# Kernel tuning notes

Hardware: AMD Instinct MI355X
Metric: run time of the kernel (lower is better)

The kernel has to match this reference:

```python
import jax, jax.numpy as jnp
import numpy as np

L, B, E, H, HID = 2048, 4, 512, 8, 2048
HD = E // H


def setup_inputs() -> dict:
    key = jax.random.key(0)
    ks = jax.random.split(key, 6)
    s = 0.02
    x = jax.random.normal(ks[0], (L, B, E), jnp.float32)
    in_proj_w = jax.random.normal(ks[1], (3 * E, E), jnp.float32) * s
    in_proj_b = jnp.zeros((3 * E,), jnp.float32)
    out_w = jax.random.normal(ks[2], (E, E), jnp.float32) * s
    out_b = jnp.zeros((E,), jnp.float32)
    w1 = jax.random.normal(ks[3], (HID, E), jnp.float32) * s  # torch Linear: (out, in)
    b1 = jnp.zeros((HID,), jnp.float32)
    w2 = jax.random.normal(ks[4], (E, HID), jnp.float32) * s
    b2 = jnp.zeros((E,), jnp.float32)
    ln_g = jnp.ones((E,), jnp.float32)
    ln_b = jnp.zeros((E,), jnp.float32)
    return {"x": x, "in_proj_w": in_proj_w, "in_proj_b": in_proj_b,
            "out_w": out_w, "out_b": out_b, "w1": w1, "b1": b1,
            "w2": w2, "b2": b2, "ln_g": ln_g, "ln_b": ln_b}


def _pos_encoding(S, Emb, dtype):
    # even i: sin((t+1) * 10000^(-i/E)); odd i: cos((t+1) * 10000^(-(i+1)/E))
    t = jnp.arange(S, dtype=dtype)[:, None]
    i = jnp.arange(Emb, dtype=dtype)[None, :]
    even = jnp.sin((t + 1.0) * jnp.power(10000.0, -i / Emb))
    odd = jnp.cos((t + 1.0) * jnp.power(10000.0, -(i + 1.0) / Emb))
    return jnp.where(jnp.arange(Emb)[None, :] % 2 == 0, even, odd)  # (S, Emb)


def _layernorm(x, g, b, eps=1e-5):
    mu = jnp.mean(x, axis=-1, keepdims=True)
    var = jnp.mean(jnp.square(x - mu), axis=-1, keepdims=True)
    return (x - mu) * jax.lax.rsqrt(var + eps) * g + b


def _mha(x, in_proj_w, in_proj_b, out_w, out_b):
    # x: (L, B, E); self-attention, torch MultiheadAttention semantics
    qkv = jnp.einsum('lbe,fe->lbf', x, in_proj_w) + in_proj_b
    q, k, v = jnp.split(qkv, 3, axis=-1)
    q = q.reshape(L, B, H, HD)
    k = k.reshape(L, B, H, HD)
    v = v.reshape(L, B, H, HD)
    scores = jnp.einsum('lbhd,mbhd->bhlm', q, k) / np.sqrt(HD).astype(np.float32)
    attn = jax.nn.softmax(scores, axis=-1)
    o = jnp.einsum('bhlm,mbhd->lbhd', attn, v).reshape(L, B, E)
    return jnp.einsum('lbe,fe->lbf', o, out_w) + out_b


def reference(x, in_proj_w, in_proj_b, out_w, out_b, w1, b1, w2, b2, ln_g, ln_b):
    # positional encoding: varies along dim1, broadcasts along dim0 (as in source)
    pe = _pos_encoding(x.shape[1], x.shape[2], x.dtype)  # (B, E)
    x = x + pe[None, :, :]
    # Post-Norm path
    x = _layernorm(_mha(x, in_proj_w, in_proj_b, out_w, out_b) + x, ln_g, ln_b)
    h = jax.nn.gelu(jnp.einsum('lbe,he->lbh', x, w1) + b1, approximate=False)
    ff = jnp.einsum('lbh,eh->lbe', h, w2) + b2
    x = _layernorm(ff + x, ln_g, ln_b)
    return x
```

## Files before the change

kernel.cpp:

```cpp
#include <hip/hip_runtime.h>

typedef unsigned short u16;
typedef unsigned int   u32;
typedef u16  u16x2 __attribute__((ext_vector_type(2)));
typedef u16  u16x4 __attribute__((ext_vector_type(4)));
typedef u16  u16x8 __attribute__((ext_vector_type(8)));
typedef short s8v  __attribute__((ext_vector_type(8)));
typedef float f4v  __attribute__((ext_vector_type(4)));
typedef u32  u32x2 __attribute__((ext_vector_type(2)));
typedef u32  u32x4 __attribute__((ext_vector_type(4)));

#define L_SEQ 2048
#define B_SZ  4
#define E_DIM 512
#define H_CNT 8
#define HD    64
#define HID   2048
#define M_ROWS (L_SEQ * B_SZ)
#define QSCALE 0.18033688011112042f

__device__ __forceinline__ u16 f2b(float f) {
    unsigned u = __builtin_bit_cast(unsigned, f);
    u += 0x7fffu + ((u >> 16) & 1u);
    return (u16)(u >> 16);
}
__device__ __forceinline__ float b2f(u16 u) {
    u32 x = ((u32)u) << 16; return __builtin_bit_cast(float, x);
}
#if defined(__has_builtin)
#if __has_builtin(__builtin_amdgcn_cvt_pk_bf16_f32)
#define HAVE_PK_BF16 1
#endif
#if __has_builtin(__builtin_amdgcn_rcpf)
#define HAVE_RCPF 1
#endif
#endif
__device__ __forceinline__ u32 pk_trunc(float a, float b) {
#ifdef HAVE_PK_BF16
    typedef __bf16 bf2 __attribute__((ext_vector_type(2)));
    bf2 r = __builtin_amdgcn_cvt_pk_bf16_f32(a, b);
    return __builtin_bit_cast(u32, r);
#else
    u32 ua = __builtin_bit_cast(u32, a), ub = __builtin_bit_cast(u32, b);
    return (ua >> 16) | (ub & 0xffff0000u);
#endif
}
__device__ __forceinline__ float frcp(float x) {
#ifdef HAVE_RCPF
    return __builtin_amdgcn_rcpf(x);
#else
    return 1.0f / x;
#endif
}
__device__ __forceinline__ void gload_lds16(const u16* g, u16* l) {
    __builtin_amdgcn_global_load_lds((__attribute__((address_space(1))) void*)(u16*)g,
                                     (__attribute__((address_space(3))) void*)l, 16, 0, 0);
}
__device__ __forceinline__ float gelu_f(float v) {
    float y2 = v * (1.5957691216f + 0.0713548576f * v * v);
    return v / (1.0f + __expf(-y2));
}

__global__ __launch_bounds__(256) void pe_tab_k(float* __restrict__ pet) {
    int i = blockIdx.x * 256 + threadIdx.x;
    int e = i & (E_DIM - 1);
    float t = (float)(i >> 9) + 1.0f;
    int ee = (e & 1) ? (e + 1) : e;
    float w = exp2f((-(float)ee / 512.0f) * 13.287712379549449f);
    pet[i] = (e & 1) ? cosf(t * w) : sinf(t * w);
}

__global__ __launch_bounds__(256) void pe_add_k(const float* __restrict__ x,
                                                const float* __restrict__ pet,
                                                u16* __restrict__ xpb) {
    int idx = (blockIdx.x * 256 + threadIdx.x) * 4;
    f4v v = *(const f4v*)(x + idx);
    f4v p = *(const f4v*)(pet + (idx & 2047));
    u16x4 o;
#pragma unroll
    for (int i = 0; i < 4; ++i) o[i] = f2b(v[i] + p[i]);
    *(u16x4*)(xpb + idx) = o;
}

__global__ __launch_bounds__(256) void conv4_k(const float* __restrict__ s1, u16* __restrict__ d1, int n1,
                                               const float* __restrict__ s2, u16* __restrict__ d2, int n2,
                                               const float* __restrict__ s3, u16* __restrict__ d3, int n3,
                                               const float* __restrict__ s4, u16* __restrict__ d4) {
    int o = (blockIdx.x * 256 + threadIdx.x) * 4;
    const float* s; u16* d;
    if (o < n1) { s = s1; d = d1; }
    else { o -= n1;
        if (o < n2) { s = s2; d = d2; }
        else { o -= n2;
            if (o < n3) { s = s3; d = d3; }
            else { o -= n3; s = s4; d = d4; } } }
    f4v v = *(const f4v*)(s + o);
    u16x4 q;
#pragma unroll
    for (int i = 0; i < 4; ++i) q[i] = f2b(v[i]);
    *(u16x4*)(d + o) = q;
}

template <int NP, bool WRITEF, bool WRITEB>
__global__ __launch_bounds__(256)
void ln_c(const u16* __restrict__ p0, const u16* __restrict__ p1,
          const u16* __restrict__ p2, const u16* __restrict__ p3,
          const float* __restrict__ bias, const u16* __restrict__ resid,
          const float* __restrict__ gw, const float* __restrict__ bw,
          float* __restrict__ outF, u16* __restrict__ outB) {
    int wave = threadIdx.x >> 6, lane = threadIdx.x & 63;
    size_t row = (size_t)blockIdx.x * 4 + wave;
    size_t off = row * E_DIM + lane * 8;
    u16x8 rv = *(const u16x8*)(resid + off);
    f4v a, b;
#pragma unroll
    for (int i = 0; i < 4; ++i) { a[i] = b2f(rv[i]); b[i] = b2f(rv[i + 4]); }
    a += *(const f4v*)(bias + lane * 8);
    b += *(const f4v*)(bias + lane * 8 + 4);
    const u16* ps[4] = {p0, p1, p2, p3};
#pragma unroll
    for (int z = 0; z < NP; ++z) {
        u16x8 t = *(const u16x8*)(ps[z] + off);
#pragma unroll
        for (int i = 0; i < 4; ++i) { a[i] += b2f(t[i]); b[i] += b2f(t[i + 4]); }
    }
    float s = (a[0] + a[1]) + (a[2] + a[3]) + (b[0] + b[1]) + (b[2] + b[3]);
#pragma unroll
    for (int o = 1; o < 64; o <<= 1) s += __shfl_xor(s, o, 64);
    float mu = s * (1.0f / E_DIM);
    float q = 0.f;
#pragma unroll
    for (int i = 0; i < 4; ++i) { float d = a[i] - mu; q += d * d; }
#pragma unroll
    for (int i = 0; i < 4; ++i) { float d = b[i] - mu; q += d * d; }
#pragma unroll
    for (int o = 1; o < 64; o <<= 1) q += __shfl_xor(q, o, 64);
    float rstd = rsqrtf(q * (1.0f / E_DIM) + 1e-5f);
    f4v g0 = *(const f4v*)(gw + lane * 8), g1 = *(const f4v*)(gw + lane * 8 + 4);
    f4v w0 = *(const f4v*)(bw + lane * 8), w1 = *(const f4v*)(bw + lane * 8 + 4);
    f4v y0, y1;
#pragma unroll
    for (int i = 0; i < 4; ++i) { y0[i] = (a[i] - mu) * rstd * g0[i] + w0[i];
                                  y1[i] = (b[i] - mu) * rstd * g1[i] + w1[i]; }
    if (WRITEF) {
        *(f4v*)(outF + off)     = y0;
        *(f4v*)(outF + off + 4) = y1;
    }
    if (WRITEB) {
        u16x8 o;
#pragma unroll
        for (int i = 0; i < 4; ++i) { o[i] = f2b(y0[i]); o[i + 4] = f2b(y1[i]); }
        *(u16x8*)(outB + off) = o;
    }
}

__global__ __launch_bounds__(256) void transpose_v_k(const u16* __restrict__ vb,
                                                     u16* __restrict__ vt) {
    __shared__ __align__(16) u16 T[64 * 66];
    int t = threadIdx.x;
    int lt = blockIdx.x, bh = blockIdx.y;
    const u16* src = vb + (size_t)bh * (L_SEQ * HD) + (size_t)lt * 64 * HD;
    int lr = t >> 2, d0 = (t & 3) * 16;
    s8v va = *(const s8v*)(src + lr * HD + d0);
    s8v vb8 = *(const s8v*)(src + lr * HD + d0 + 8);
#pragma unroll
    for (int c = 0; c < 4; ++c) {
        u16x2 p0; p0[0] = (u16)va[c * 2]; p0[1] = (u16)va[c * 2 + 1];
        u16x2 p1; p1[0] = (u16)vb8[c * 2]; p1[1] = (u16)vb8[c * 2 + 1];
        *(u16x2*)(&T[lr * 66 + d0 + c * 2])     = p0;
        *(u16x2*)(&T[lr * 66 + d0 + 8 + c * 2]) = p1;
    }
    __syncthreads();
    int d = t >> 2, l0 = (t & 3) * 16;
    u16 tmp[16];
#pragma unroll
    for (int i = 0; i < 16; ++i) tmp[i] = T[(l0 + i) * 66 + d];
    u16* dst = vt + (size_t)bh * (L_SEQ * HD) + (size_t)d * L_SEQ + lt * 64 + l0;
    u16x8 o0, o1;
#pragma unroll
    for (int i = 0; i < 8; ++i) { o0[i] = tmp[i]; o1[i] = tmp[8 + i]; }
    *(u16x8*)dst       = o0;
    *(u16x8*)(dst + 8) = o1;
}

template <int MODE, int NT>
__global__ __launch_bounds__(256, 4)
void gemm_bt(const u16* __restrict__ A, const u16* __restrict__ Bw,
             const float* __restrict__ bias, int M, int N, int K,
             u16* __restrict__ outB,
             u16* __restrict__ oq, u16* __restrict__ okk, u16* __restrict__ ov) {
    __shared__ __align__(16) u16 As[2][128 * 32];
    __shared__ __align__(16) u16 Bs[2][128 * 32];
    const int tid = threadIdx.x;
    const int wave = tid >> 6, lane = tid & 63;
    const int col = lane & 15, quad = lane >> 4;
    const int n = blockIdx.x;
    const int xcd = n & 7, loc = n >> 3;
    const int mpx = (M / 128) >> 3;
    const int bm = (xcd * mpx + loc / NT) * 128;
    const int bn = (loc % NT) * 128;
    const int wm = (wave >> 1) * 64, wn = (wave & 1) * 64;
    f4v acc[4][4] = {};
    const int srow = wave * 16 + (lane >> 2);
    const int soff = (lane & 3) * 8;
    const u16* Ag = A + (size_t)(bm + srow) * K + soff;
    const u16* Bg = Bw + (size_t)(bn + srow) * K + soff;
    const int wo = wave * 512;
    gload_lds16(Ag,                  &As[0][wo]);
    gload_lds16(Ag + (size_t)64 * K, &As[0][wo + 2048]);
    gload_lds16(Bg,                  &Bs[0][wo]);
    gload_lds16(Bg + (size_t)64 * K, &Bs[0][wo + 2048]);
    const int nit = K >> 5;
    for (int t = 0; t < nit; ++t) {
        const int cur = t & 1, nxt = cur ^ 1;
        __syncthreads();
        if (t + 1 < nit) {
            const int kc = (t + 1) * 32;
            gload_lds16(Ag + kc,                  &As[nxt][wo]);
            gload_lds16(Ag + (size_t)64 * K + kc, &As[nxt][wo + 2048]);
            gload_lds16(Bg + kc,                  &Bs[nxt][wo]);
            gload_lds16(Bg + (size_t)64 * K + kc, &Bs[nxt][wo + 2048]);
        }
        s8v af[4], bf[4];
#pragma unroll
        for (int i = 0; i < 4; ++i) af[i] = *(const s8v*)(&As[cur][(wm + i * 16 + col) * 32 + quad * 8]);
#pragma unroll
        for (int j = 0; j < 4; ++j) bf[j] = *(const s8v*)(&Bs[cur][(wn + j * 16 + col) * 32 + quad * 8]);
#pragma unroll
        for (int i = 0; i < 4; ++i)
#pragma unroll
            for (int j = 0; j < 4; ++j)
                acc[i][j] = __builtin_amdgcn_mfma_f32_16x16x32_bf16(af[i], bf[j], acc[i][j], 0, 0, 0);
    }
#pragma unroll
    for (int j = 0; j < 4; ++j) {
        int gn = bn + wn + j * 16 + col;
        float bv = bias[gn];
        int which = gn >> 9, hh = (gn >> 6) & 7, d = gn & 63;
        u16* dst = (MODE == 0) ? ((which == 0) ? oq : ((which == 1) ? okk : ov)) : outB;
        float qs = (MODE == 0 && which == 0) ? QSCALE : 1.0f;
#pragma unroll
        for (int i = 0; i < 4; ++i) {
            int gm0 = bm + wm + i * 16 + quad * 4;
#pragma unroll
            for (int r = 0; r < 4; ++r) {
                float v = acc[i][j][r] + bv;
                int m = gm0 + r;
                if (MODE == 2) {
                    outB[(size_t)m * N + gn] = f2b(gelu_f(v));
                } else {
                    int l = m >> 2, bb = m & 3;
                    dst[((size_t)(bb * H_CNT + hh) * L_SEQ + l) * HD + d] = f2b(v * qs);
                }
            }
        }
    }
}

__global__ __launch_bounds__(256, 4)
void gemm_ks(const u16* __restrict__ A, const u16* __restrict__ Bw,
             int N, int K, int Kper,
             u16* __restrict__ q0, u16* __restrict__ q1) {
    __shared__ __align__(16) u16 As[2][128 * 32];
    __shared__ __align__(16) u16 Bs[2][128 * 32];
    const int tid = threadIdx.x;
    const int wave = tid >> 6, lane = tid & 63;
    const int col = lane & 15, quad = lane >> 4;
    const int n = blockIdx.x;
    const int xcd = n & 7, loc = n >> 3;
    const int bn = (loc & 3) * 128;
    const int bm = (xcd * 8 + ((loc >> 2) & 7)) * 128;
    const int kz = loc >> 5;
    u16* pz = kz ? q1 : q0;
    const int wm = (wave >> 1) * 64, wn = (wave & 1) * 64;
    f4v acc[4][4] = {};
    const int srow = wave * 16 + (lane >> 2);
    const int soff = (lane & 3) * 8;
    const u16* Ag = A + (size_t)(bm + srow) * K + kz * Kper + soff;
    const u16* Bg = Bw + (size_t)(bn + srow) * K + kz * Kper + soff;
    const int wo = wave * 512;
    gload_lds16(Ag,                  &As[0][wo]);
    gload_lds16(Ag + (size_t)64 * K, &As[0][wo + 2048]);
    gload_lds16(Bg,                  &Bs[0][wo]);
    gload_lds16(Bg + (size_t)64 * K, &Bs[0][wo + 2048]);
    const int nit = Kper >> 5;
    for (int t = 0; t < nit; ++t) {
        const int cur = t & 1, nxt = cur ^ 1;
        __syncthreads();
        if (t + 1 < nit) {
            const int kc = (t + 1) * 32;
            gload_lds16(Ag + kc,                  &As[nxt][wo]);
            gload_lds16(Ag + (size_t)64 * K + kc, &As[nxt][wo + 2048]);
            gload_lds16(Bg + kc,                  &Bs[nxt][wo]);
            gload_lds16(Bg + (size_t)64 * K + kc, &Bs[nxt][wo + 2048]);
        }
        s8v af[4], bf[4];
#pragma unroll
        for (int i = 0; i < 4; ++i) af[i] = *(const s8v*)(&As[cur][(wm + i * 16 + col) * 32 + quad * 8]);
#pragma unroll
        for (int j = 0; j < 4; ++j) bf[j] = *(const s8v*)(&Bs[cur][(wn + j * 16 + col) * 32 + quad * 8]);
#pragma unroll
        for (int i = 0; i < 4; ++i)
#pragma unroll
            for (int j = 0; j < 4; ++j)
                acc[i][j] = __builtin_amdgcn_mfma_f32_16x16x32_bf16(af[i], bf[j], acc[i][j], 0, 0, 0);
    }
#pragma unroll
    for (int j = 0; j < 4; ++j) {
        int gn = bn + wn + j * 16 + col;
#pragma unroll
        for (int i = 0; i < 4; ++i) {
            int m0 = bm + wm + i * 16 + quad * 4;
#pragma unroll
            for (int r = 0; r < 4; ++r)
                pz[(size_t)(m0 + r) * N + gn] = f2b(acc[i][j][r]);
        }
    }
}

__global__ __launch_bounds__(256, 4)
void attn_k(const u16* __restrict__ qg, const u16* __restrict__ kg,
            const u16* __restrict__ vtg, u16* __restrict__ og) {
    __shared__ __align__(16) u16 Ks[2][2][64 * 32];
    __shared__ __align__(16) u16 Vs[2][2][64 * 32];
    const int tid = threadIdx.x;
    const int wave = tid >> 6, lane = tid & 63;
    const int col = lane & 15, quad = lane >> 4;
    const int flat = blockIdx.x;
    const int xcd = flat & 7, loc = flat >> 3;
    const int bh = xcd * 4 + (loc >> 4);
    const int qc = loc & 15;
    const size_t base = (size_t)bh * (L_SEQ * HD);
    s8v qf[2][2];
#pragma unroll
    for (int t = 0; t < 2; ++t) {
        const int qrow = qc * 128 + wave * 32 + t * 16 + col;
#pragma unroll
        for (int hh = 0; hh < 2; ++hh)
            qf[t][hh] = *(const s8v*)(qg + base + (size_t)qrow * HD + hh * 32 + quad * 8);
    }
    f4v oa[2][4] = {};
    float ls0 = 0.f, ls1 = 0.f;
    const int h = wave & 1, r0 = (wave >> 1) * 16;
    const int srow = lane >> 2, c = lane & 3;
    const int cp = c ^ ((srow >> 1) & 3);
    const int sig = ((srow >> 2) << 3) + ((r0 >> 4) << 2) + (srow & 3);
    const u16* Kg = kg + base + (size_t)sig * HD + h * 32 + cp * 8;
    const u16* Vg = vtg + base + (size_t)(r0 + srow) * L_SEQ + h * 32 + cp * 8;
    {
        gload_lds16(Kg,                      &Ks[0][h][r0 * 32]);
        gload_lds16(Kg + (size_t)32 * HD,    &Ks[0][h][(r0 + 32) * 32]);
        gload_lds16(Vg,                      &Vs[0][h][r0 * 32]);
        gload_lds16(Vg + (size_t)32 * L_SEQ, &Vs[0][h][(r0 + 32) * 32]);
    }
    const int perm = (col >> 1) & 3;
    for (int it = 0; it < 32; ++it) {
        const int cur = it & 1, nxt = cur ^ 1;
        __syncthreads();
        if (it + 1 < 32) {
            const int kv0 = (it + 1) * 64;
            gload_lds16(Kg + (size_t)kv0 * HD,         &Ks[nxt][h][r0 * 32]);
            gload_lds16(Kg + (size_t)(kv0 + 32) * HD,  &Ks[nxt][h][(r0 + 32) * 32]);
            gload_lds16(Vg + kv0,                      &Vs[nxt][h][r0 * 32]);
            gload_lds16(Vg + kv0 + (size_t)32 * L_SEQ, &Vs[nxt][h][(r0 + 32) * 32]);
        }
        f4v st[2][4];
#pragma unroll
        for (int j = 0; j < 4; ++j) {
            s8v k0 = *(const s8v*)(&Ks[cur][0][(j * 16 + col) * 32 + ((quad ^ perm) * 8)]);
            s8v k1 = *(const s8v*)(&Ks[cur][1][(j * 16 + col) * 32 + ((quad ^ perm) * 8)]);
#pragma unroll
            for (int t = 0; t < 2; ++t) {
                f4v z = {};
                z = __builtin_amdgcn_mfma_f32_16x16x32_bf16(k0, qf[t][0], z, 0, 0, 0);
                z = __builtin_amdgcn_mfma_f32_16x16x32_bf16(k1, qf[t][1], z, 0, 0, 0);
                st[t][j] = z;
            }
        }
        u32 pk[2][4][2];
#pragma unroll
        for (int t = 0; t < 2; ++t)
#pragma unroll
            for (int j = 0; j < 4; ++j) {
                f4v p;
#pragma unroll
                for (int r = 0; r < 4; ++r) p[r] = __builtin_amdgcn_exp2f(st[t][j][r]);
                float psum = (p[0] + p[1]) + (p[2] + p[3]);
                if (t == 0) ls0 += psum; else ls1 += psum;
                pk[t][j][0] = pk_trunc(p[0], p[1]);
                pk[t][j][1] = pk_trunc(p[2], p[3]);
            }
#pragma unroll
        for (int c2 = 0; c2 < 2; ++c2) {
            s8v pf[2];
#pragma unroll
            for (int t = 0; t < 2; ++t) {
                u32x4 q4 = {pk[t][2 * c2][0], pk[t][2 * c2][1],
                            pk[t][2 * c2 + 1][0], pk[t][2 * c2 + 1][1]};
                pf[t] = __builtin_bit_cast(s8v, q4);
            }
#pragma unroll
            for (int dj = 0; dj < 4; ++dj) {
                s8v vf = *(const s8v*)(&Vs[cur][c2][(dj * 16 + col) * 32 + ((quad ^ perm) * 8)]);
#pragma unroll
                for (int t = 0; t < 2; ++t)
                    oa[t][dj] = __builtin_amdgcn_mfma_f32_16x16x32_bf16(pf[t], vf, oa[t][dj], 0, 0, 0);
            }
        }
    }
    ls0 += __shfl_xor(ls0, 16, 64); ls0 += __shfl_xor(ls0, 32, 64);
    ls1 += __shfl_xor(ls1, 16, 64); ls1 += __shfl_xor(ls1, 32, 64);
    const int b = bh >> 3, hd = bh & 7;
#pragma unroll
    for (int t = 0; t < 2; ++t)
#pragma unroll
        for (int r = 0; r < 4; ++r) {
            float lv = __shfl(t == 0 ? ls0 : ls1, quad * 4 + r, 64);
            float inv = frcp(lv);
            int lrow = qc * 128 + wave * 32 + t * 16 + quad * 4 + r;
            size_t mrow = (size_t)(lrow * 4 + b) * E_DIM + hd * HD;
#pragma unroll
            for (int dj = 0; dj < 4; ++dj)
                og[mrow + dj * 16 + col] = f2b(oa[t][dj][r] * inv);
        }
}

extern "C" void kernel_launch(void* const* d_in, const int* in_sizes, int n_in,
                              void* d_out, int out_size, void* d_ws, size_t ws_size,
                              hipStream_t stream) {
    const float* x     = (const float*)d_in[0];
    const float* w_qkv = (const float*)d_in[1];
    const float* b_qkv = (const float*)d_in[2];
    const float* w_out = (const float*)d_in[3];
    const float* b_out = (const float*)d_in[4];
    const float* w1    = (const float*)d_in[5];
    const float* b1    = (const float*)d_in[6];
    const float* w2    = (const float*)d_in[7];
    const float* b2    = (const float*)d_in[8];
    const float* ln_g  = (const float*)d_in[9];
    const float* ln_b  = (const float*)d_in[10];

    char* ws = (char*)d_ws;
    u16*   WQKV = (u16*)(ws + 0);
    u16*   WOUT = (u16*)(ws + 1572864);
    u16*   W1B  = (u16*)(ws + 2097152);
    u16*   W2B  = (u16*)(ws + 4194304);
    u16*   XPB  = (u16*)(ws + 6291456);
    u16*   QB   = (u16*)(ws + 14680064);
    u16*   KB   = (u16*)(ws + 23068672);
    u16*   VB   = (u16*)(ws + 31457280);
    u16*   VT   = (u16*)(ws + 39845888);
    float* PET  = (float*)(ws + 82837504);
    u16*   OB   = VB;
    u16*   OP0  = (u16*)(ws + 48234496);
    u16*   OP1  = (u16*)(ws + 56623104);
    u16*   X3B  = QB;
    u16*   HB   = (u16*)(ws + 48234496);
    u16*   FP0  = XPB;
    u16*   FP1  = KB;

    pe_tab_k<<<8, 256, 0, stream>>>(PET);
    pe_add_k<<<4096, 256, 0, stream>>>(x, PET, XPB);
    conv4_k<<<3072, 256, 0, stream>>>(w_qkv, WQKV, 3 * E_DIM * E_DIM,
                                      w_out, WOUT, E_DIM * E_DIM,
                                      w1, W1B, HID * E_DIM,
                                      w2, W2B);
    gemm_bt<0, 12><<<768, 256, 0, stream>>>(XPB, WQKV, b_qkv, M_ROWS, 3 * E_DIM, E_DIM,
                                            nullptr, QB, KB, VB);
    transpose_v_k<<<dim3(32, 32), 256, 0, stream>>>(VB, VT);
    attn_k<<<512, 256, 0, stream>>>(QB, KB, VT, OB);
    gemm_ks<<<512, 256, 0, stream>>>(OB, WOUT, E_DIM, E_DIM, 256, OP0, OP1);
    ln_c<2, false, true><<<2048, 256, 0, stream>>>(OP0, OP1, nullptr, nullptr,
                                                   b_out, XPB, ln_g, ln_b, nullptr, X3B);
    gemm_bt<2, 16><<<1024, 256, 0, stream>>>(X3B, W1B, b1, M_ROWS, HID, E_DIM,
                                             HB, nullptr, nullptr, nullptr);
    gemm_ks<<<512, 256, 0, stream>>>(HB, W2B, E_DIM, HID, 1024, FP0, FP1);
    ln_c<2, true, false><<<2048, 256, 0, stream>>>(FP0, FP1, nullptr, nullptr,
                                                   b2, X3B, ln_g, ln_b, (float*)d_out, nullptr);
}
```

Before: 243.4 us.

## Add 256x256 eight-wave triple-buffered GEMM for FFN layers with 4-way split-K

Introduces a new 512-thread GEMM kernel with 256x256 output tiles, triple-buffered direct global-to-LDS loads with swizzling, and MFMA priority hints. It replaces the FFN up-projection (with fused GELU) and the down-projection, which now uses a 4-way K split whose partial sums are combined in the layernorm kernel. The aim is more data reuse per tile and better overlap of loads with compute. The cost is larger LDS use (96KB dynamic), fewer blocks, and an extra partial buffer to read in the final layernorm.

Result: slower. 249.5 us (+2.5%).

```diff
diff --git a/kernel.cpp b/kernel.cpp
--- a/kernel.cpp
+++ b/kernel.cpp
@@ -318,6 +318,103 @@
     }
 }
 
+#define G8_STAGE(Ad, Bd, kf)                                                           \
+    {                                                                                  \
+        _Pragma("unroll")                                                              \
+        for (int s = 0; s < 2; ++s) {                                                  \
+            const int q = (s * 8 + wave) * 64 + lane;                                  \
+            const int rho = q >> 2;                                                    \
+            gload_lds16(A  + (size_t)(bm + rho) * Ka + (kf) + gsw, (Ad) + q * 8);      \
+            gload_lds16(Bw + (size_t)(bn + rho) * Kb + (kf) + gsw, (Bd) + q * 8);      \
+        }                                                                              \
+    }
+
+#define G8_COMPUTE(Ab_, Bb_)                                                           \
+    {                                                                                  \
+        s8v bfr[4];                                                                    \
+        _Pragma("unroll")                                                              \
+        for (int j = 0; j < 4; ++j) {                                                  \
+            const int rB = wc * 64 + j * 16 + col;                                     \
+            bfr[j] = *(const s8v*)((Bb_) + rB * 32 + ((quad ^ ((rB >> 1) & 3)) * 8));  \
+        }                                                                              \
+        _Pragma("unroll")                                                              \
+        for (int ih = 0; ih < 2; ++ih) {                                               \
+            s8v afr[4];                                                                \
+            _Pragma("unroll")                                                          \
+            for (int i = 0; i < 4; ++i) {                                              \
+                const int rA = wr * 128 + (ih * 4 + i) * 16 + col;                     \
+                afr[i] = *(const s8v*)((Ab_) + rA * 32 + ((quad ^ ((rA >> 1) & 3)) * 8)); \
+            }                                                                          \
+            __builtin_amdgcn_s_setprio(1);                                             \
+            _Pragma("unroll")                                                          \
+            for (int i = 0; i < 4; ++i)                                                \
+                _Pragma("unroll")                                                      \
+                for (int j = 0; j < 4; ++j)                                            \
+                    acc[ih * 4 + i][j] = __builtin_amdgcn_mfma_f32_16x16x32_bf16(afr[i], bfr[j], acc[ih * 4 + i][j], 0, 0, 0); \
+            __builtin_amdgcn_s_setprio(0);                                             \
+        }                                                                              \
+    }
+
+template <int MODE, int NTL, int KZL>
+__global__ __launch_bounds__(512, 2)
+void gemm8(const u16* __restrict__ A, const u16* __restrict__ Bw,
+           const float* __restrict__ bias, int Ka, int Kb, int N,
+           u16* __restrict__ o0, u16* __restrict__ o1,
+           u16* __restrict__ o2, u16* __restrict__ o3) {
+    extern __shared__ __align__(16) u16 LDS[];
+    const int tid = threadIdx.x;
+    const int wave = tid >> 6, lane = tid & 63;
+    const int col = lane & 15, quad = lane >> 4;
+    const int wr = wave >> 2, wc = wave & 3;
+    const int n = blockIdx.x;
+    const int xcd = n & 7, loc = n >> 3;
+    const int mt = xcd * 4 + (loc & 3);
+    const int rest = loc >> 2;
+    const int nt = (NTL == 1) ? 0 : (rest % NTL);
+    const int kz = (KZL == 1) ? 0 : (rest / NTL);
+    const int bm = mt * 256, bn = nt * 256;
+    const int koff0 = kz * 512;
+    const int gsw = ((lane & 3) ^ ((lane >> 3) & 3)) * 8;
+    f4v acc[8][4] = {};
+    u16* A0 = LDS;          u16* B0 = LDS + 8192;
+    u16* A1 = LDS + 16384;  u16* B1 = LDS + 24576;
+    u16* A2 = LDS + 32768;  u16* B2 = LDS + 40960;
+    G8_STAGE(A0, B0, koff0);
+    G8_STAGE(A1, B1, koff0 + 32);
+    asm volatile("s_waitcnt vmcnt(4)" ::: "memory");
+    __builtin_amdgcn_s_barrier();
+    __builtin_amdgcn_sched_barrier(0);
+    for (int t = 0; t < 14; ++t) {
+        G8_STAGE(A2, B2, koff0 + (t + 2) * 32);
+        G8_COMPUTE(A0, B0);
+        asm volatile("s_waitcnt vmcnt(4)" ::: "memory");
+        __builtin_amdgcn_s_barrier();
+        __builtin_amdgcn_sched_barrier(0);
+        u16* ta = A0; A0 = A1; A1 = A2; A2 = ta;
+        u16* tb = B0; B0 = B1; B1 = B2; B2 = tb;
+    }
+    G8_COMPUTE(A0, B0);
+    asm volatile("s_waitcnt vmcnt(0)" ::: "memory");
+    __builtin_amdgcn_s_barrier();
+    __builtin_amdgcn_sched_barrier(0);
+    G8_COMPUTE(A1, B1);
+    u16* outp = (MODE == 2) ? o0 : ((kz == 0) ? o0 : (kz == 1) ? o1 : (kz == 2) ? o2 : o3);
+#pragma unroll
+    for (int j = 0; j < 4; ++j) {
+        const int gn = bn + wc * 64 + j * 16 + col;
+        const float bv = (MODE == 2) ? bias[gn] : 0.0f;
+#pragma unroll
+        for (int i = 0; i < 8; ++i) {
+            const int m0 = bm + wr * 128 + i * 16 + quad * 4;
+#pragma unroll
+            for (int r = 0; r < 4; ++r) {
+                float v = acc[i][j][r] + bv;
+                outp[(size_t)(m0 + r) * N + gn] = f2b(MODE == 2 ? gelu_f(v) : v);
+            }
+        }
+    }
+}
+
 __global__ __launch_bounds__(256, 4)
 void attn_k(const u16* __restrict__ qg, const u16* __restrict__ kg,
             const u16* __restrict__ vtg, u16* __restrict__ og) {
@@ -458,6 +555,17 @@
     u16*   HB   = (u16*)(ws + 48234496);
     u16*   FP0  = XPB;
     u16*   FP1  = KB;
+    u16*   FP2  = VB;
+    u16*   FP3  = VT;
+
+    static bool attr_done = false;
+    if (!attr_done) {
+        hipFuncSetAttribute((const void*)gemm8<2, 8, 1>,
+                            hipFuncAttributeMaxDynamicSharedMemorySize, 98304);
+        hipFuncSetAttribute((const void*)gemm8<3, 2, 4>,
+                            hipFuncAttributeMaxDynamicSharedMemorySize, 98304);
+        attr_done = true;
+    }
 
     pe_tab_k<<<8, 256, 0, stream>>>(PET);
     pe_add_k<<<4096, 256, 0, stream>>>(x, PET, XPB);
@@ -472,9 +580,10 @@
     gemm_ks<<<512, 256, 0, stream>>>(OB, WOUT, E_DIM, E_DIM, 256, OP0, OP1);
     ln_c<2, false, true><<<2048, 256, 0, stream>>>(OP0, OP1, nullptr, nullptr,
                                                    b_out, XPB, ln_g, ln_b, nullptr, X3B);
-    gemm_bt<2, 16><<<1024, 256, 0, stream>>>(X3B, W1B, b1, M_ROWS, HID, E_DIM,
-                                             HB, nullptr, nullptr, nullptr);
-    gemm_ks<<<512, 256, 0, stream>>>(HB, W2B, E_DIM, HID, 1024, FP0, FP1);
-    ln_c<2, true, false><<<2048, 256, 0, stream>>>(FP0, FP1, nullptr, nullptr,
+    gemm8<2, 8, 1><<<256, 512, 98304, stream>>>(X3B, W1B, b1, E_DIM, E_DIM, HID,
+                                                HB, nullptr, nullptr, nullptr);
+    gemm8<3, 2, 4><<<256, 512, 98304, stream>>>(HB, W2B, nullptr, HID, HID, E_DIM,
+                                                FP0, FP1, FP2, FP3);
+    ln_c<4, true, false><<<2048, 256, 0, stream>>>(FP0, FP1, FP2, FP3,
                                                    b2, X3B, ln_g, ln_b, (float*)d_out, nullptr);
 }
```

## Split attention KV range across two wave groups and combine partials in LDS

Applied to the files above, without the earlier changes.

The attention kernel now launches 512 threads per block. Two groups of four waves each process half of the 2048 keys for the same 128 query rows, each with its own double-buffered K/V tiles in LDS. This doubles the waves working on each block to hide latency and halves the per-wave serial loop. The partial outputs and row sums from group 1 are stored to LDS, reusing the K/V buffers, and group 0 adds them before normalizing and writing. The cost is twice the LDS footprint, an extra barrier and the combine step, and fewer resident blocks per CU.

Result: no change. 242.2 us (-0.5%).

```diff
diff --git a/kernel.cpp b/kernel.cpp
--- a/kernel.cpp
+++ b/kernel.cpp
@@ -318,13 +318,14 @@
     }
 }
 
-__global__ __launch_bounds__(256, 4)
+__global__ __launch_bounds__(512, 4)
 void attn_k(const u16* __restrict__ qg, const u16* __restrict__ kg,
             const u16* __restrict__ vtg, u16* __restrict__ og) {
-    __shared__ __align__(16) u16 Ks[2][2][64 * 32];
-    __shared__ __align__(16) u16 Vs[2][2][64 * 32];
+    __shared__ __align__(16) u16 KV[2][2][2][2][64 * 32];
+    __shared__ float LSB[2][256];
     const int tid = threadIdx.x;
     const int wave = tid >> 6, lane = tid & 63;
+    const int grp = wave >> 2, w4 = wave & 3;
     const int col = lane & 15, quad = lane >> 4;
     const int flat = blockIdx.x;
     const int xcd = flat & 7, loc = flat >> 3;
@@ -334,41 +335,41 @@
     s8v qf[2][2];
 #pragma unroll
     for (int t = 0; t < 2; ++t) {
-        const int qrow = qc * 128 + wave * 32 + t * 16 + col;
+        const int qrow = qc * 128 + w4 * 32 + t * 16 + col;
 #pragma unroll
         for (int hh = 0; hh < 2; ++hh)
             qf[t][hh] = *(const s8v*)(qg + base + (size_t)qrow * HD + hh * 32 + quad * 8);
     }
     f4v oa[2][4] = {};
     float ls0 = 0.f, ls1 = 0.f;
-    const int h = wave & 1, r0 = (wave >> 1) * 16;
+    const int h = w4 & 1, r0 = (w4 >> 1) * 16;
     const int srow = lane >> 2, c = lane & 3;
     const int cp = c ^ ((srow >> 1) & 3);
     const int sig = ((srow >> 2) << 3) + ((r0 >> 4) << 2) + (srow & 3);
-    const u16* Kg = kg + base + (size_t)sig * HD + h * 32 + cp * 8;
-    const u16* Vg = vtg + base + (size_t)(r0 + srow) * L_SEQ + h * 32 + cp * 8;
+    const u16* Kg = kg + base + (size_t)(sig + grp * 1024) * HD + h * 32 + cp * 8;
+    const u16* Vg = vtg + base + (size_t)(r0 + srow) * L_SEQ + grp * 1024 + h * 32 + cp * 8;
     {
-        gload_lds16(Kg,                      &Ks[0][h][r0 * 32]);
-        gload_lds16(Kg + (size_t)32 * HD,    &Ks[0][h][(r0 + 32) * 32]);
-        gload_lds16(Vg,                      &Vs[0][h][r0 * 32]);
-        gload_lds16(Vg + (size_t)32 * L_SEQ, &Vs[0][h][(r0 + 32) * 32]);
+        gload_lds16(Kg,                      &KV[grp][0][0][h][r0 * 32]);
+        gload_lds16(Kg + (size_t)32 * HD,    &KV[grp][0][0][h][(r0 + 32) * 32]);
+        gload_lds16(Vg,                      &KV[grp][1][0][h][r0 * 32]);
+        gload_lds16(Vg + (size_t)32 * L_SEQ, &KV[grp][1][0][h][(r0 + 32) * 32]);
     }
     const int perm = (col >> 1) & 3;
-    for (int it = 0; it < 32; ++it) {
+    for (int it = 0; it < 16; ++it) {
         const int cur = it & 1, nxt = cur ^ 1;
         __syncthreads();
-        if (it + 1 < 32) {
+        if (it + 1 < 16) {
             const int kv0 = (it + 1) * 64;
-            gload_lds16(Kg + (size_t)kv0 * HD,         &Ks[nxt][h][r0 * 32]);
-            gload_lds16(Kg + (size_t)(kv0 + 32) * HD,  &Ks[nxt][h][(r0 + 32) * 32]);
-            gload_lds16(Vg + kv0,                      &Vs[nxt][h][r0 * 32]);
-            gload_lds16(Vg + kv0 + (size_t)32 * L_SEQ, &Vs[nxt][h][(r0 + 32) * 32]);
+            gload_lds16(Kg + (size_t)kv0 * HD,         &KV[grp][0][nxt][h][r0 * 32]);
+            gload_lds16(Kg + (size_t)(kv0 + 32) * HD,  &KV[grp][0][nxt][h][(r0 + 32) * 32]);
+            gload_lds16(Vg + kv0,                      &KV[grp][1][nxt][h][r0 * 32]);
+            gload_lds16(Vg + kv0 + (size_t)32 * L_SEQ, &KV[grp][1][nxt][h][(r0 + 32) * 32]);
         }
         f4v st[2][4];
 #pragma unroll
         for (int j = 0; j < 4; ++j) {
-            s8v k0 = *(const s8v*)(&Ks[cur][0][(j * 16 + col) * 32 + ((quad ^ perm) * 8)]);
-            s8v k1 = *(const s8v*)(&Ks[cur][1][(j * 16 + col) * 32 + ((quad ^ perm) * 8)]);
+            s8v k0 = *(const s8v*)(&KV[grp][0][cur][0][(j * 16 + col) * 32 + ((quad ^ perm) * 8)]);
+            s8v k1 = *(const s8v*)(&KV[grp][0][cur][1][(j * 16 + col) * 32 + ((quad ^ perm) * 8)]);
 #pragma unroll
             for (int t = 0; t < 2; ++t) {
                 f4v z = {};
@@ -401,7 +402,7 @@
             }
 #pragma unroll
             for (int dj = 0; dj < 4; ++dj) {
-                s8v vf = *(const s8v*)(&Vs[cur][c2][(dj * 16 + col) * 32 + ((quad ^ perm) * 8)]);
+                s8v vf = *(const s8v*)(&KV[grp][1][cur][c2][(dj * 16 + col) * 32 + ((quad ^ perm) * 8)]);
 #pragma unroll
                 for (int t = 0; t < 2; ++t)
                     oa[t][dj] = __builtin_amdgcn_mfma_f32_16x16x32_bf16(pf[t], vf, oa[t][dj], 0, 0, 0);
@@ -410,19 +411,40 @@
     }
     ls0 += __shfl_xor(ls0, 16, 64); ls0 += __shfl_xor(ls0, 32, 64);
     ls1 += __shfl_xor(ls1, 16, 64); ls1 += __shfl_xor(ls1, 32, 64);
-    const int b = bh >> 3, hd = bh & 7;
-#pragma unroll
-    for (int t = 0; t < 2; ++t)
-#pragma unroll
-        for (int r = 0; r < 4; ++r) {
-            float lv = __shfl(t == 0 ? ls0 : ls1, quad * 4 + r, 64);
-            float inv = frcp(lv);
-            int lrow = qc * 128 + wave * 32 + t * 16 + quad * 4 + r;
-            size_t mrow = (size_t)(lrow * 4 + b) * E_DIM + hd * HD;
+    float* cmb = (float*)&KV[1][0][0][0][0];
+    const int slot = w4 * 64 + lane;
+    if (grp == 1) {
+#pragma unroll
+        for (int t = 0; t < 2; ++t)
 #pragma unroll
             for (int dj = 0; dj < 4; ++dj)
-                og[mrow + dj * 16 + col] = f2b(oa[t][dj][r] * inv);
-        }
+                *(f4v*)(cmb + ((size_t)(t * 4 + dj) * 256 + slot) * 4) = oa[t][dj];
+        LSB[0][slot] = ls0;
+        LSB[1][slot] = ls1;
+    }
+    __syncthreads();
+    if (grp == 0) {
+#pragma unroll
+        for (int t = 0; t < 2; ++t)
+#pragma unroll
+            for (int dj = 0; dj < 4; ++dj)
+                oa[t][dj] += *(const f4v*)(cmb + ((size_t)(t * 4 + dj) * 256 + slot) * 4);
+        ls0 += LSB[0][slot];
+        ls1 += LSB[1][slot];
+        const int b = bh >> 3, hd = bh & 7;
+#pragma unroll
+        for (int t = 0; t < 2; ++t)
+#pragma unroll
+            for (int r = 0; r < 4; ++r) {
+                float lv = __shfl(t == 0 ? ls0 : ls1, quad * 4 + r, 64);
+                float inv = frcp(lv);
+                int lrow = qc * 128 + w4 * 32 + t * 16 + quad * 4 + r;
+                size_t mrow = (size_t)(lrow * 4 + b) * E_DIM + hd * HD;
+#pragma unroll
+                for (int dj = 0; dj < 4; ++dj)
+                    og[mrow + dj * 16 + col] = f2b(oa[t][dj][r] * inv);
+            }
+    }
 }
 
 extern "C" void kernel_launch(void* const* d_in, const int* in_sizes, int n_in,
@@ -468,7 +490,7 @@
     gemm_bt<0, 12><<<768, 256, 0, stream>>>(XPB, WQKV, b_qkv, M_ROWS, 3 * E_DIM, E_DIM,
                                             nullptr, QB, KB, VB);
     transpose_v_k<<<dim3(32, 32), 256, 0, stream>>>(VB, VT);
-    attn_k<<<512, 256, 0, stream>>>(QB, KB, VT, OB);
+    attn_k<<<512, 512, 0, stream>>>(QB, KB, VT, OB);
     gemm_ks<<<512, 256, 0, stream>>>(OB, WOUT, E_DIM, E_DIM, 256, OP0, OP1);
     ln_c<2, false, true><<<2048, 256, 0, stream>>>(OP0, OP1, nullptr, nullptr,
                                                    b_out, XPB, ln_g, ln_b, nullptr, X3B);
```
